# Kernel tuning notes

Measured on AMD Instinct MI355X. Metric: run time of the kernel, lower is better.

## Reference

```python
import jax, jax.numpy as jnp
import numpy as np

T = 36  # num_frames


def box_cxcywh_to_xyxy(b):
    cx, cy, w, h = jnp.split(b, 4, axis=-1)
    return jnp.concatenate([cx - 0.5 * w, cy - 0.5 * h, cx + 0.5 * w, cy + 0.5 * h], axis=-1)


def multi_iou(b1, b2):
    # b1: [Q,1,T,4], b2: [1,N,T,4], xyxy -> iou [Q,N,T]
    lt = jnp.maximum(b1[..., :2], b2[..., :2])
    rb = jnp.minimum(b1[..., 2:], b2[..., 2:])
    wh = jnp.clip(rb - lt, 0.0)
    inter = wh[..., 0] * wh[..., 1]
    a1 = (b1[..., 2] - b1[..., 0]) * (b1[..., 3] - b1[..., 1])
    a2 = (b2[..., 2] - b2[..., 0]) * (b2[..., 3] - b2[..., 1])
    union = a1 + a2 - inter
    return inter / union


def setup_inputs() -> dict:
    key = jax.random.key(0)
    k1, k2, k3, k4, k5, k6 = jax.random.split(key, 6)
    Q, N, C = 2048, 128, 42
    return {
        "pred_logits": jax.random.normal(k1, (T * Q, C), dtype=jnp.float32),
        "pred_boxes": jax.random.uniform(k2, (T * Q, 4), dtype=jnp.float32),
        "tgt_labels": jax.random.randint(k3, (N * T,), 0, C - 1),
        "tgt_boxes": jax.random.uniform(k4, (N * T, 4), dtype=jnp.float32),
        "tgt_valid": jax.random.randint(k5, (N * T,), 0, 2, dtype=jnp.int32),
        "tgt_original_valid": jax.random.randint(k6, (N * T,), 0, 2, dtype=jnp.int32),
    }


def reference(pred_logits, pred_boxes, tgt_labels, tgt_boxes, tgt_valid, tgt_original_valid):
    # Cost-matrix computation of SoftMaxHungarianMatcher (cost_class=cost_bbox=cost_giou=1,
    # use_giou=False, use_l1_distance_sum=False). The scipy linear_sum_assignment step is
    # CPU-serial / non-tensor and excluded; output is the [Q,N] cost fed to it.
    C = pred_logits.shape[-1]
    Q = pred_logits.shape[0] // T
    N = tgt_labels.shape[0] // T
    num_classes = C - 1  # background index

    probs = jax.nn.softmax(pred_logits, axis=-1).reshape(T, Q, C).transpose(1, 0, 2)  # [Q,T,C]
    boxes = pred_boxes.reshape(T, Q, 4).transpose(1, 0, 2)                            # [Q,T,4]
    tboxes = tgt_boxes.reshape(N, T, 4)
    valid = tgt_valid.reshape(N, T).astype(probs.dtype)                               # [N,T]
    ovalid = tgt_original_valid.reshape(N, T)
    ids = jnp.where(ovalid == 0, num_classes, tgt_labels.reshape(N, T))               # [N,T]

    denom = valid.sum(-1)  # [N] (per-instance count of valid frames)

    # class cost: -mean_t p(q, t, ids[n,t]) over valid frames
    gathered = probs[:, jnp.arange(T)[None, :], ids]                                  # [Q,N,T]
    class_cost = -(gathered * valid).sum(-1) / denom                                  # [Q,N]

    # bbox L1 cost: mean over (valid frames, 4 coords)
    l1 = jnp.abs(boxes[:, None] - tboxes[None]).mean(-1)                              # [Q,N,T]
    bbox_cost = (l1 * valid).sum(-1) / denom                                          # [Q,N]

    # IoU cost: -mean_t iou over valid frames
    iou = multi_iou(box_cxcywh_to_xyxy(boxes)[:, None], box_cxcywh_to_xyxy(tboxes)[None])
    iou_cost = -(iou * valid).sum(-1) / denom                                         # [Q,N]

    return class_cost + bbox_cost + iou_cost
```

## Files before the change

### kernel.cpp

```cpp
#include <hip/hip_runtime.h>
#include <hip/hip_bf16.h>


constexpr int T = 36;
constexpr int Q = 2048;
constexpr int C = 42;
constexpr int N = 128;

__global__ __launch_bounds__(256) void softmax_transpose_kernel(
    const float* __restrict__ logits, float* __restrict__ P2) {
  constexpr int QB = 64;
  constexpr int LDS_STRIDE = C + 1;
  const int t = blockIdx.y;
  const int q0 = blockIdx.x * QB;
  const int tid = threadIdx.x;

  __shared__ float tile[QB * LDS_STRIDE];
  __shared__ float rmax[QB];
  __shared__ float rinv[QB];

  const float* src = logits + ((size_t)t * Q + q0) * C;
  for (int i = tid; i < QB * C; i += 256) {
    int r = i / C, c = i % C;
    tile[r * LDS_STRIDE + c] = src[i];
  }
  __syncthreads();

  if (tid < QB) {
    const float* row = tile + tid * LDS_STRIDE;
    float m = -1e30f;
    for (int c = 0; c < C; ++c) m = fmaxf(m, row[c]);
    float s = 0.f;
    for (int c = 0; c < C; ++c) s += __expf(row[c] - m);
    rmax[tid] = m;
    rinv[tid] = 1.f / s;
  }
  __syncthreads();

  for (int i = tid; i < QB * C; i += 256) {
    int c = i >> 6;
    int r = i & 63;
    float v = __expf(tile[r * LDS_STRIDE + c] - rmax[r]) * rinv[r];
    P2[(size_t)(t * C + c) * Q + q0 + r] = v;
  }
}

__global__ __launch_bounds__(256) void cost_kernel(
    const float* __restrict__ P2, const float* __restrict__ pred_boxes,
    const int* __restrict__ labels, const float* __restrict__ tboxes,
    const int* __restrict__ valid, const int* __restrict__ ovalid,
    float* __restrict__ out) {
  constexpr int NB = 4;
  constexpr int RES_STRIDE = NB + 1;

  const int q0 = blockIdx.x * 64;
  const int n0 = blockIdx.y * NB;
  const int tid = threadIdx.x;
  const int lane = tid & 63;
  const int sub = tid >> 6;
  const int q = q0 + lane;

  __shared__ float4 s_tb[NB * T];
  __shared__ int s_idv[NB * T];
  __shared__ float s_rden[NB];
  __shared__ float s_res[64 * RES_STRIDE];

  for (int i = tid; i < NB * T; i += 256) {
    int n = n0 + i / T;
    int t = i % T;
    int g = n * T + t;
    s_idv[i] = ((ovalid[g] == 0) ? (C - 1) : labels[g]) | (valid[g] << 8);
    s_tb[i] = ((const float4*)tboxes)[g];
  }
  if (tid < NB) {
    int n = n0 + tid;
    int s = 0;
    for (int t = 0; t < T; ++t) s += valid[n * T + t];
    s_rden[tid] = 1.f / (float)s;
  }
  __syncthreads();

  float acc = 0.f;
  const float* probs_base = P2 + q;

  for (int t = 0; t < T; ++t) {
    int pk = s_idv[sub * T + t];
    if (pk & 0x100) {
      float4 pb = ((const float4*)pred_boxes)[t * Q + q];
      float4 tb = s_tb[sub * T + t];
      int id = pk & 0xff;
      float p = probs_base[(size_t)(t * C + id) * Q];

      float l1 = 0.25f * (fabsf(pb.x - tb.x) + fabsf(pb.y - tb.y) +
                          fabsf(pb.z - tb.z) + fabsf(pb.w - tb.w));
      float px1 = pb.x - 0.5f * pb.z, py1 = pb.y - 0.5f * pb.w;
      float px2 = pb.x + 0.5f * pb.z, py2 = pb.y + 0.5f * pb.w;
      float tx1 = tb.x - 0.5f * tb.z, ty1 = tb.y - 0.5f * tb.w;
      float tx2 = tb.x + 0.5f * tb.z, ty2 = tb.y + 0.5f * tb.w;
      float iw = fmaxf(fminf(px2, tx2) - fmaxf(px1, tx1), 0.f);
      float ih = fmaxf(fminf(py2, ty2) - fmaxf(py1, ty1), 0.f);
      float inter = iw * ih;
      float uni = pb.z * pb.w + tb.z * tb.w - inter;
      acc += l1 - p - inter / uni;
    }
  }

  s_res[lane * RES_STRIDE + sub] = acc * s_rden[sub];
  __syncthreads();

  if (tid < 64) {
    float4 o;
    o.x = s_res[tid * RES_STRIDE + 0];
    o.y = s_res[tid * RES_STRIDE + 1];
    o.z = s_res[tid * RES_STRIDE + 2];
    o.w = s_res[tid * RES_STRIDE + 3];
    *(float4*)(out + (size_t)(q0 + tid) * N + n0) = o;
  }
}

extern "C" void kernel_launch(void* const* d_in, const int* in_sizes, int n_in,
                              void* d_out, int out_size, void* d_ws, size_t ws_size,
                              hipStream_t stream) {
  const float* logits = (const float*)d_in[0];
  const float* pboxes = (const float*)d_in[1];
  const int* labels = (const int*)d_in[2];
  const float* tboxes = (const float*)d_in[3];
  const int* valid = (const int*)d_in[4];
  const int* ovalid = (const int*)d_in[5];
  float* out = (float*)d_out;

  float* P2 = (float*)d_ws;

  dim3 g1(Q / 64, T);
  softmax_transpose_kernel<<<g1, 256, 0, stream>>>(logits, P2);

  dim3 g2(Q / 64, N / 4);
  cost_kernel<<<g2, 256, 0, stream>>>(P2, pboxes, labels, tboxes, valid, ovalid, out);
}
```

Baseline: 88.11 us.

## Parallelize softmax reduction, stage pred boxes in LDS, make cost loop branchless

The softmax kernel now spreads each row's max and sum reductions over all four wavefronts instead of one, and stores the exponentials in LDS so they are not recomputed on the write-out pass. The cost kernel loads the block's predicted boxes into LDS once and reuses them across the four target instances. Its per-frame loop is fully unrolled and branch-free: it multiplies by the valid flag and reads the packed flag with readfirstlane. This trades skipped work on invalid frames for no divergence and more ILP, and adds 36 KB of LDS per block, which may cap occupancy despite the launch-bounds hint.

```diff
diff --git a/kernel.cpp b/kernel.cpp
--- a/kernel.cpp
+++ b/kernel.cpp
@@ -10,42 +10,60 @@
 __global__ __launch_bounds__(256) void softmax_transpose_kernel(
     const float* __restrict__ logits, float* __restrict__ P2) {
   constexpr int QB = 64;
-  constexpr int LDS_STRIDE = C + 1;
+  constexpr int LS = C + 1;
+
+  __shared__ float tile[QB * LS];
+  __shared__ float s_max[4 * QB];
+  __shared__ float s_sum[4 * QB];
+  __shared__ float s_rinv[QB];
+
   const int t = blockIdx.y;
   const int q0 = blockIdx.x * QB;
   const int tid = threadIdx.x;
 
-  __shared__ float tile[QB * LDS_STRIDE];
-  __shared__ float rmax[QB];
-  __shared__ float rinv[QB];
-
   const float* src = logits + ((size_t)t * Q + q0) * C;
   for (int i = tid; i < QB * C; i += 256) {
     int r = i / C, c = i % C;
-    tile[r * LDS_STRIDE + c] = src[i];
+    tile[r * LS + c] = src[i];
   }
   __syncthreads();
 
-  if (tid < QB) {
-    const float* row = tile + tid * LDS_STRIDE;
-    float m = -1e30f;
-    for (int c = 0; c < C; ++c) m = fmaxf(m, row[c]);
-    float s = 0.f;
-    for (int c = 0; c < C; ++c) s += __expf(row[c] - m);
-    rmax[tid] = m;
-    rinv[tid] = 1.f / s;
+  const int part = tid >> 6;
+  const int row = tid & 63;
+  const int c0 = (part < 2) ? part * 11 : 22 + (part - 2) * 10;
+  const int c1 = (part < 2) ? c0 + 11 : c0 + 10;
+
+  float m = -1e30f;
+  for (int c = c0; c < c1; ++c) m = fmaxf(m, tile[row * LS + c]);
+  s_max[part * QB + row] = m;
+  __syncthreads();
+
+  m = fmaxf(fmaxf(s_max[row], s_max[QB + row]),
+            fmaxf(s_max[2 * QB + row], s_max[3 * QB + row]));
+  float s = 0.f;
+  for (int c = c0; c < c1; ++c) {
+    float e = __expf(tile[row * LS + c] - m);
+    tile[row * LS + c] = e;
+    s += e;
+  }
+  s_sum[part * QB + row] = s;
+  __syncthreads();
+
+  if (part == 0) {
+    float stot = s_sum[row] + s_sum[QB + row] + s_sum[2 * QB + row] +
+                 s_sum[3 * QB + row];
+    s_rinv[row] = 1.f / stot;
   }
   __syncthreads();
 
   for (int i = tid; i < QB * C; i += 256) {
     int c = i >> 6;
     int r = i & 63;
-    float v = __expf(tile[r * LDS_STRIDE + c] - rmax[r]) * rinv[r];
-    P2[(size_t)(t * C + c) * Q + q0 + r] = v;
+    P2[(size_t)(t * C + c) * Q + q0 + r] = tile[r * LS + c] * s_rinv[r];
   }
 }
 
-__global__ __launch_bounds__(256) void cost_kernel(
+__global__ __launch_bounds__(256, 4) void cost_kernel(
     const float* __restrict__ P2, const float* __restrict__ pred_boxes,
     const int* __restrict__ labels, const float* __restrict__ tboxes,
     const int* __restrict__ valid, const int* __restrict__ ovalid,
@@ -60,11 +78,16 @@
   const int sub = tid >> 6;
   const int q = q0 + lane;
 
+  __shared__ float4 s_pb[T * 64];
   __shared__ float4 s_tb[NB * T];
   __shared__ int s_idv[NB * T];
   __shared__ float s_rden[NB];
   __shared__ float s_res[64 * RES_STRIDE];
 
+  for (int i = tid; i < T * 64; i += 256) {
+    int t = i >> 6, l = i & 63;
+    s_pb[t * 64 + l] = ((const float4*)pred_boxes)[t * Q + q0 + l];
+  }
   for (int i = tid; i < NB * T; i += 256) {
     int n = n0 + i / T;
     int t = i % T;
@@ -83,26 +106,26 @@
   float acc = 0.f;
   const float* probs_base = P2 + q;
 
+#pragma unroll
   for (int t = 0; t < T; ++t) {
-    int pk = s_idv[sub * T + t];
-    if (pk & 0x100) {
-      float4 pb = ((const float4*)pred_boxes)[t * Q + q];
-      float4 tb = s_tb[sub * T + t];
-      int id = pk & 0xff;
-      float p = probs_base[(size_t)(t * C + id) * Q];
+    int pk = __builtin_amdgcn_readfirstlane(s_idv[sub * T + t]);
+    int id = pk & 0xff;
+    float v = (float)(pk >> 8);
+    float p = probs_base[(size_t)(t * C + id) * Q];
+    float4 pb = s_pb[t * 64 + lane];
+    float4 tb = s_tb[sub * T + t];
 
-      float l1 = 0.25f * (fabsf(pb.x - tb.x) + fabsf(pb.y - tb.y) +
-                          fabsf(pb.z - tb.z) + fabsf(pb.w - tb.w));
-      float px1 = pb.x - 0.5f * pb.z, py1 = pb.y - 0.5f * pb.w;
-      float px2 = pb.x + 0.5f * pb.z, py2 = pb.y + 0.5f * pb.w;
-      float tx1 = tb.x - 0.5f * tb.z, ty1 = tb.y - 0.5f * tb.w;
-      float tx2 = tb.x + 0.5f * tb.z, ty2 = tb.y + 0.5f * tb.w;
-      float iw = fmaxf(fminf(px2, tx2) - fmaxf(px1, tx1), 0.f);
-      float ih = fmaxf(fminf(py2, ty2) - fmaxf(py1, ty1), 0.f);
-      float inter = iw * ih;
-      float uni = pb.z * pb.w + tb.z * tb.w - inter;
-      acc += l1 - p - inter / uni;
-    }
+    float l1 = 0.25f * (fabsf(pb.x - tb.x) + fabsf(pb.y - tb.y) +
+                        fabsf(pb.z - tb.z) + fabsf(pb.w - tb.w));
+    float px1 = pb.x - 0.5f * pb.z, py1 = pb.y - 0.5f * pb.w;
+    float px2 = pb.x + 0.5f * pb.z, py2 = pb.y + 0.5f * pb.w;
+    float tx1 = tb.x - 0.5f * tb.z, ty1 = tb.y - 0.5f * tb.w;
+    float tx2 = tb.x + 0.5f * tb.z, ty2 = tb.y + 0.5f * tb.w;
+    float iw = fmaxf(fminf(px2, tx2) - fmaxf(px1, tx1), 0.f);
+    float ih = fmaxf(fminf(py2, ty2) - fmaxf(py1, ty1), 0.f);
+    float inter = iw * ih;
+    float uni = pb.z * pb.w + tb.z * tb.w - inter;
+    acc += v * (l1 - p - inter / uni);
   }
 
   s_res[lane * RES_STRIDE + sub] = acc * s_rden[sub];
```

Result: slower. 94.46 us (+7.2%).
